# Performance work log

Measured on AMD Instinct MI355X. Metric: run time of the kernel, lower is better.

The kernel has to match this reference:

```python
import jax, jax.numpy as jnp
import numpy as np

N_NODES = 100000
N_RELS = 4
N_EDGES = 250000  # per relation
D = 128


def setup_inputs() -> dict:
    key = jax.random.key(0)
    ks = jax.random.split(key, 7)
    scale = 1.0 / np.sqrt(D)  # xavier-like scaling for stability
    x = jax.random.normal(ks[0], (N_NODES, D), dtype=jnp.float32)
    weight = jax.random.normal(ks[1], (N_RELS, D, D), dtype=jnp.float32) * scale
    conv_bias = jax.random.normal(ks[2], (N_RELS, D), dtype=jnp.float32) * 0.1
    loop_weight = jax.random.normal(ks[3], (D, D), dtype=jnp.float32) * scale
    node_bias = jax.random.normal(ks[4], (1, D), dtype=jnp.float32) * 0.1
    src = jax.random.randint(ks[5], (N_RELS, N_EDGES), 0, N_NODES)
    dst = jax.random.randint(ks[6], (N_RELS, N_EDGES), 0, N_NODES)
    return {"x": x, "weight": weight, "conv_bias": conv_bias,
            "loop_weight": loop_weight, "node_bias": node_bias,
            "src": src, "dst": dst}


def reference(x, weight, conv_bias, loop_weight, node_bias, src, dst):
    N = x.shape[0]

    def per_rel(s, d, W, b):
        # GraphConv(norm='right'): sum src feats into dst, divide by in-degree (clamped to 1),
        # then matmul weight (aggregate-first since in_feat == out_feat), add bias, activation.
        msg = jax.ops.segment_sum(x[s], d, num_segments=N)              # [N, D]
        deg = jax.ops.segment_sum(jnp.ones(s.shape, x.dtype), d, num_segments=N)
        h = (msg / jnp.maximum(deg, 1.0)[:, None]) @ W + b              # [N, D]
        return jax.nn.relu(h)

    hs = jax.vmap(per_rel)(src, dst, weight, conv_bias)                 # [R, N, D]
    h = hs.mean(axis=0)                                                 # HeteroGraphConv aggregate='mean'
    h = h * jax.nn.sigmoid(h)                                           # GLU(tile(h, 2)) == SiLU(h)
    h = h + x @ loop_weight + node_bias                                  # self-loop + ntype bias
    return jax.nn.relu(h)                                                # dropout=0 (eval)
```

## Files before the change

kernel.cpp:

```cpp
#include <hip/hip_runtime.h>
#include <hip/hip_bf16.h>

#define N_NODES 100000
#define N_RELS  4
#define N_EDGES 250000
#define TOTAL_E (N_RELS * N_EDGES)
#define NR      (N_RELS * N_NODES)
#define D       128

typedef __attribute__((ext_vector_type(8))) short bf16x8;
typedef __attribute__((ext_vector_type(4))) float f32x4;

__device__ __forceinline__ float b2f(short u) {
    unsigned int x = ((unsigned int)(unsigned short)u) << 16;
    return __builtin_bit_cast(float, x);
}
__device__ __forceinline__ unsigned short f2b(float f) {
    unsigned int u = __builtin_bit_cast(unsigned int, f);
    return (unsigned short)((u + 0x7fffu + ((u >> 16) & 1u)) >> 16);
}

__global__ __launch_bounds__(256) void hist_kernel(
    const int* __restrict__ dst, int* __restrict__ deg, int total)
{
    int i = blockIdx.x * 256 + threadIdx.x;
    if (i >= total) return;
    int rel = i / N_EDGES;
    atomicAdd(&deg[rel * N_NODES + dst[i]], 1);
}

__global__ __launch_bounds__(256) void scan1_kernel(
    const int* __restrict__ in, int* __restrict__ out,
    int* __restrict__ aux, int n)
{
    __shared__ int s[256];
    int t = threadIdx.x;
    int base = blockIdx.x * 1024 + t * 4;
    int v[4];
    int sum = 0;
    #pragma unroll
    for (int j = 0; j < 4; ++j) {
        v[j] = (base + j < n) ? in[base + j] : 0;
        sum += v[j];
    }
    s[t] = sum;
    for (int off = 1; off < 256; off <<= 1) {
        __syncthreads();
        int u = (t >= off) ? s[t - off] : 0;
        __syncthreads();
        s[t] += u;
    }
    __syncthreads();
    int excl = (t > 0) ? s[t - 1] : 0;
    #pragma unroll
    for (int j = 0; j < 4; ++j) {
        if (base + j < n) out[base + j] = excl;
        excl += v[j];
    }
    if (t == 255) aux[blockIdx.x] = s[255];
}

__global__ __launch_bounds__(512) void scan2_kernel(int* __restrict__ aux, int n)
{
    __shared__ int s[512];
    int t = threadIdx.x;
    s[t] = (t < n) ? aux[t] : 0;
    for (int off = 1; off < 512; off <<= 1) {
        __syncthreads();
        int u = (t >= off) ? s[t - off] : 0;
        __syncthreads();
        s[t] += u;
    }
    __syncthreads();
    int excl = (t > 0) ? s[t - 1] : 0;
    if (t < n) aux[t] = excl;
}

__global__ __launch_bounds__(256) void addoff_kernel(
    int* __restrict__ off, int* __restrict__ cursor,
    const int* __restrict__ aux, int n)
{
    int i = blockIdx.x * 256 + threadIdx.x;
    if (i >= n) return;
    int v = off[i] + aux[i >> 10];
    off[i] = v;
    cursor[i] = v;
}

__global__ __launch_bounds__(256) void fill_kernel(
    const int* __restrict__ dst, const int* __restrict__ src,
    int* __restrict__ cursor, int* __restrict__ sorted_src, int total)
{
    int i = blockIdx.x * 256 + threadIdx.x;
    if (i >= total) return;
    int rel = i / N_EDGES;
    int pos = atomicAdd(&cursor[rel * N_NODES + dst[i]], 1);
    sorted_src[pos] = src[i];
}

__global__ __launch_bounds__(256) void convert_x_kernel(
    const float* __restrict__ x, unsigned short* __restrict__ xb, int total8)
{
    int i = blockIdx.x * 256 + threadIdx.x;
    if (i >= total8) return;
    float4 v0 = *reinterpret_cast<const float4*>(x + (size_t)i * 8);
    float4 v1 = *reinterpret_cast<const float4*>(x + (size_t)i * 8 + 4);
    bf16x8 o;
    o[0] = (short)f2b(v0.x); o[1] = (short)f2b(v0.y);
    o[2] = (short)f2b(v0.z); o[3] = (short)f2b(v0.w);
    o[4] = (short)f2b(v1.x); o[5] = (short)f2b(v1.y);
    o[6] = (short)f2b(v1.z); o[7] = (short)f2b(v1.w);
    *reinterpret_cast<bf16x8*>(xb + (size_t)i * 8) = o;
}

__global__ __launch_bounds__(256) void convert_w_kernel(
    const float* __restrict__ weight,
    const float* __restrict__ loop_w,
    unsigned short* __restrict__ wT)
{
    int i = blockIdx.x * 256 + threadIdx.x;
    if (i >= 5 * D * D) return;
    int mat = i >> 14;
    int n   = (i >> 7) & 127;
    int k   = i & 127;
    const float* srcm = (mat < 4) ? (weight + (size_t)mat * D * D) : loop_w;
    wT[i] = f2b(srcm[k * D + n]);
}

__global__ __launch_bounds__(256) void fused_gemm_mfma(
    const unsigned short* __restrict__ xb,
    const unsigned short* __restrict__ wT,
    const float* __restrict__ conv_bias,
    const float* __restrict__ node_bias,
    const int* __restrict__ deg,
    const int* __restrict__ off,
    const int* __restrict__ sorted_src,
    float* __restrict__ out)
{
    __shared__ __align__(16) unsigned char sIn[32 * 256];

    const int tid  = threadIdx.x;
    const int row0 = blockIdx.x * 32;
    const int wid  = tid >> 6;
    const int lane = tid & 63;
    const int l15  = lane & 15;
    const int l4   = lane >> 4;
    const int swA  = (l15 & 7) << 4;

    const int gr = tid >> 3;
    const int gc = tid & 7;
    const int gsw = (gr & 7) << 4;

    f32x4 acc_mean[2][2];
    f32x4 acc_self[2][2];
    #pragma unroll
    for (int m = 0; m < 2; ++m)
        #pragma unroll
        for (int n = 0; n < 2; ++n)
            acc_mean[m][n] = (f32x4){0.f, 0.f, 0.f, 0.f};

    for (int phase = 0; phase < 5; ++phase) {
        __syncthreads();

        if (phase < 4) {
            int node = row0 + gr;
            int dgi  = deg[phase * N_NODES + node];
            int beg  = off[phase * N_NODES + node];
            float a[16];
            #pragma unroll
            for (int j = 0; j < 16; ++j) a[j] = 0.f;
            const int* sp = sorted_src + beg;
            for (int e = 0; e < dgi; ++e) {
                const unsigned short* xp = xb + (size_t)sp[e] * D + gc * 16;
                bf16x8 v0 = *reinterpret_cast<const bf16x8*>(xp);
                bf16x8 v1 = *reinterpret_cast<const bf16x8*>(xp + 8);
                #pragma unroll
                for (int j = 0; j < 8; ++j) {
                    a[j]     += b2f(v0[j]);
                    a[8 + j] += b2f(v1[j]);
                }
            }
            float scale = 1.0f / fmaxf((float)dgi, 1.0f);
            bf16x8 o0, o1;
            #pragma unroll
            for (int j = 0; j < 8; ++j) {
                o0[j] = (short)f2b(a[j] * scale);
                o1[j] = (short)f2b(a[8 + j] * scale);
            }
            int base = gr * 256;
            *reinterpret_cast<bf16x8*>(&sIn[base + ((gc * 32) ^ gsw)])      = o0;
            *reinterpret_cast<bf16x8*>(&sIn[base + ((gc * 32 + 16) ^ gsw)]) = o1;
        } else {
            #pragma unroll
            for (int t = 0; t < 2; ++t) {
                int id = tid + t * 256;
                int r  = id >> 4;
                int kb = (id & 15) * 16;
                bf16x8 v = *reinterpret_cast<const bf16x8*>(
                    xb + (size_t)(row0 + r) * D + kb / 2);
                *reinterpret_cast<bf16x8*>(&sIn[r * 256 + (kb ^ ((r & 7) << 4))]) = v;
            }
        }
        __syncthreads();

        const unsigned short* wp = wT + (size_t)phase * D * D;
        bf16x8 bfr[2][4];
        #pragma unroll
        for (int n = 0; n < 2; ++n)
            #pragma unroll
            for (int s = 0; s < 4; ++s) {
                int col = wid * 32 + n * 16 + l15;
                bfr[n][s] = *reinterpret_cast<const bf16x8*>(
                    wp + col * D + s * 32 + l4 * 8);
            }

        f32x4 acc[2][2];
        #pragma unroll
        for (int m = 0; m < 2; ++m)
            #pragma unroll
            for (int n = 0; n < 2; ++n)
                acc[m][n] = (f32x4){0.f, 0.f, 0.f, 0.f};

        #pragma unroll
        for (int s = 0; s < 4; ++s) {
            int kb = s * 64 + l4 * 16;
            bf16x8 a0 = *reinterpret_cast<const bf16x8*>(
                &sIn[l15 * 256 + (kb ^ swA)]);
            bf16x8 a1 = *reinterpret_cast<const bf16x8*>(
                &sIn[(16 + l15) * 256 + (kb ^ swA)]);
            acc[0][0] = __builtin_amdgcn_mfma_f32_16x16x32_bf16(a0, bfr[0][s], acc[0][0], 0, 0, 0);
            acc[0][1] = __builtin_amdgcn_mfma_f32_16x16x32_bf16(a0, bfr[1][s], acc[0][1], 0, 0, 0);
            acc[1][0] = __builtin_amdgcn_mfma_f32_16x16x32_bf16(a1, bfr[0][s], acc[1][0], 0, 0, 0);
            acc[1][1] = __builtin_amdgcn_mfma_f32_16x16x32_bf16(a1, bfr[1][s], acc[1][1], 0, 0, 0);
        }

        if (phase < 4) {
            float b0 = conv_bias[phase * D + wid * 32 + l15];
            float b1 = conv_bias[phase * D + wid * 32 + 16 + l15];
            #pragma unroll
            for (int m = 0; m < 2; ++m)
                #pragma unroll
                for (int j = 0; j < 4; ++j) {
                    acc_mean[m][0][j] += 0.25f * fmaxf(acc[m][0][j] + b0, 0.f);
                    acc_mean[m][1][j] += 0.25f * fmaxf(acc[m][1][j] + b1, 0.f);
                }
        } else {
            float b0 = node_bias[wid * 32 + l15];
            float b1 = node_bias[wid * 32 + 16 + l15];
            #pragma unroll
            for (int m = 0; m < 2; ++m)
                #pragma unroll
                for (int j = 0; j < 4; ++j) {
                    acc_self[m][0][j] = acc[m][0][j] + b0;
                    acc_self[m][1][j] = acc[m][1][j] + b1;
                }
        }
    }

    #pragma unroll
    for (int m = 0; m < 2; ++m)
        #pragma unroll
        for (int n = 0; n < 2; ++n)
            #pragma unroll
            for (int j = 0; j < 4; ++j) {
                float mn = acc_mean[m][n][j];
                float sl = mn / (1.0f + __expf(-mn));
                float v  = fmaxf(sl + acc_self[m][n][j], 0.f);
                int row = row0 + m * 16 + l4 * 4 + j;
                int col = wid * 32 + n * 16 + l15;
                out[(size_t)row * D + col] = v;
            }
}

extern "C" void kernel_launch(void* const* d_in, const int* in_sizes, int n_in,
                              void* d_out, int out_size, void* d_ws, size_t ws_size,
                              hipStream_t stream) {
    const float* x         = (const float*)d_in[0];
    const float* weight    = (const float*)d_in[1];
    const float* conv_bias = (const float*)d_in[2];
    const float* loop_w    = (const float*)d_in[3];
    const float* node_bias = (const float*)d_in[4];
    const int*   src       = (const int*)d_in[5];
    const int*   dst       = (const int*)d_in[6];
    float* out = (float*)d_out;

    char* w = (char*)d_ws;
    int* deg                  = (int*)(w);
    int* off                  = (int*)(w + 1600000);
    int* cursor               = (int*)(w + 3200000);
    int* aux                  = (int*)(w + 4800000);
    int* sorted_src           = (int*)(w + 4802048);
    unsigned short* xb        = (unsigned short*)(w + 8802048);
    unsigned short* wT        = (unsigned short*)(w + 8802048 + (size_t)N_NODES * D * 2);

    const int SCAN_BLKS = (NR + 1023) / 1024;

    convert_x_kernel<<<(N_NODES * D / 8 + 255) / 256, 256, 0, stream>>>(
        x, xb, N_NODES * D / 8);
    convert_w_kernel<<<(5 * D * D + 255) / 256, 256, 0, stream>>>(
        weight, loop_w, wT);

    hipMemsetAsync(deg, 0, NR * sizeof(int), stream);
    hist_kernel<<<(TOTAL_E + 255) / 256, 256, 0, stream>>>(dst, deg, TOTAL_E);
    scan1_kernel<<<SCAN_BLKS, 256, 0, stream>>>(deg, off, aux, NR);
    scan2_kernel<<<1, 512, 0, stream>>>(aux, SCAN_BLKS);
    addoff_kernel<<<(NR + 255) / 256, 256, 0, stream>>>(off, cursor, aux, NR);
    fill_kernel<<<(TOTAL_E + 255) / 256, 256, 0, stream>>>(dst, src, cursor,
                                                           sorted_src, TOTAL_E);

    fused_gemm_mfma<<<N_NODES / 32, 256, 0, stream>>>(
        xb, wT, conv_bias, node_bias, deg, off, sorted_src, out);
}
```

Measured before the change: 355.4 us.

## Merge prep kernels, fold scan passes, and gather edges per block with LDS atomics

Folds the x/weight conversion and the degree histogram into one prep kernel. It also drops the separate second scan kernel by having each block reduce the preceding block sums itself. The fill step now packs the source index with the destination's low 5 bits. This lets the fused kernel spread a 32-node tile's edges evenly over all threads and accumulate them into an fp32 LDS tile with shared-memory atomics, replacing the per-node serial loops that suffered load imbalance. Weight fragments are now loaded from global memory inside the MFMA loop rather than hoisted, and the self-loop GEMM reads x directly from global memory. The LDS float atomics and the larger shared footprint may contend or reduce occupancy.

```diff
diff --git a/kernel.cpp b/kernel.cpp
--- a/kernel.cpp
+++ b/kernel.cpp
@@ -20,13 +20,40 @@
     return (unsigned short)((u + 0x7fffu + ((u >> 16) & 1u)) >> 16);
 }
 
-__global__ __launch_bounds__(256) void hist_kernel(
-    const int* __restrict__ dst, int* __restrict__ deg, int total)
-{
-    int i = blockIdx.x * 256 + threadIdx.x;
-    if (i >= total) return;
-    int rel = i / N_EDGES;
-    atomicAdd(&deg[rel * N_NODES + dst[i]], 1);
+#define PREP_X_BLKS 6250
+#define PREP_W_BLKS 320
+#define PREP_H_BLKS 3907
+__global__ __launch_bounds__(256) void prep_kernel(
+    const float* __restrict__ x, const float* __restrict__ weight,
+    const float* __restrict__ loop_w, const int* __restrict__ dst,
+    unsigned short* __restrict__ xb, unsigned short* __restrict__ wT,
+    int* __restrict__ deg)
+{
+    int b = blockIdx.x, t = threadIdx.x;
+    if (b < PREP_X_BLKS) {
+        int i = b * 256 + t;
+        float4 v0 = *reinterpret_cast<const float4*>(x + (size_t)i * 8);
+        float4 v1 = *reinterpret_cast<const float4*>(x + (size_t)i * 8 + 4);
+        bf16x8 o;
+        o[0] = (short)f2b(v0.x); o[1] = (short)f2b(v0.y);
+        o[2] = (short)f2b(v0.z); o[3] = (short)f2b(v0.w);
+        o[4] = (short)f2b(v1.x); o[5] = (short)f2b(v1.y);
+        o[6] = (short)f2b(v1.z); o[7] = (short)f2b(v1.w);
+        *reinterpret_cast<bf16x8*>(xb + (size_t)i * 8) = o;
+    } else if (b < PREP_X_BLKS + PREP_W_BLKS) {
+        int i = (b - PREP_X_BLKS) * 256 + t;
+        int mat = i >> 14;
+        int n   = (i >> 7) & 127;
+        int k   = i & 127;
+        const float* srcm = (mat < 4) ? (weight + (size_t)mat * D * D) : loop_w;
+        wT[i] = f2b(srcm[k * D + n]);
+    } else {
+        int i = (b - PREP_X_BLKS - PREP_W_BLKS) * 256 + t;
+        if (i < TOTAL_E) {
+            int rel = i / N_EDGES;
+            atomicAdd(&deg[rel * N_NODES + dst[i]], 1);
+        }
+    }
 }
 
 __global__ __launch_bounds__(256) void scan1_kernel(
@@ -60,71 +87,39 @@
     if (t == 255) aux[blockIdx.x] = s[255];
 }
 
-__global__ __launch_bounds__(512) void scan2_kernel(int* __restrict__ aux, int n)
-{
-    __shared__ int s[512];
-    int t = threadIdx.x;
-    s[t] = (t < n) ? aux[t] : 0;
-    for (int off = 1; off < 512; off <<= 1) {
-        __syncthreads();
-        int u = (t >= off) ? s[t - off] : 0;
-        __syncthreads();
-        s[t] += u;
-    }
-    __syncthreads();
-    int excl = (t > 0) ? s[t - 1] : 0;
-    if (t < n) aux[t] = excl;
-}
-
-__global__ __launch_bounds__(256) void addoff_kernel(
+__global__ __launch_bounds__(256) void addoff2_kernel(
     int* __restrict__ off, int* __restrict__ cursor,
     const int* __restrict__ aux, int n)
 {
-    int i = blockIdx.x * 256 + threadIdx.x;
-    if (i >= n) return;
-    int v = off[i] + aux[i >> 10];
-    off[i] = v;
-    cursor[i] = v;
-}
-
-__global__ __launch_bounds__(256) void fill_kernel(
+    __shared__ int sred[256];
+    int c = blockIdx.x, t = threadIdx.x;
+    int part = 0;
+    for (int j = t; j < c; j += 256) part += aux[j];
+    sred[t] = part;
+    for (int o = 128; o > 0; o >>= 1) {
+        __syncthreads();
+        if (t < o) sred[t] += sred[t + o];
+    }
+    __syncthreads();
+    int S = sred[0];
+    int base = c * 1024 + t * 4;
+    #pragma unroll
+    for (int j = 0; j < 4; ++j) {
+        int i = base + j;
+        if (i < n) { int v = off[i] + S; off[i] = v; cursor[i] = v; }
+    }
+}
+
+__global__ __launch_bounds__(256) void fill_pack_kernel(
     const int* __restrict__ dst, const int* __restrict__ src,
-    int* __restrict__ cursor, int* __restrict__ sorted_src, int total)
+    int* __restrict__ cursor, unsigned int* __restrict__ sorted_pack, int total)
 {
     int i = blockIdx.x * 256 + threadIdx.x;
     if (i >= total) return;
     int rel = i / N_EDGES;
-    int pos = atomicAdd(&cursor[rel * N_NODES + dst[i]], 1);
-    sorted_src[pos] = src[i];
-}
-
-__global__ __launch_bounds__(256) void convert_x_kernel(
-    const float* __restrict__ x, unsigned short* __restrict__ xb, int total8)
-{
-    int i = blockIdx.x * 256 + threadIdx.x;
-    if (i >= total8) return;
-    float4 v0 = *reinterpret_cast<const float4*>(x + (size_t)i * 8);
-    float4 v1 = *reinterpret_cast<const float4*>(x + (size_t)i * 8 + 4);
-    bf16x8 o;
-    o[0] = (short)f2b(v0.x); o[1] = (short)f2b(v0.y);
-    o[2] = (short)f2b(v0.z); o[3] = (short)f2b(v0.w);
-    o[4] = (short)f2b(v1.x); o[5] = (short)f2b(v1.y);
-    o[6] = (short)f2b(v1.z); o[7] = (short)f2b(v1.w);
-    *reinterpret_cast<bf16x8*>(xb + (size_t)i * 8) = o;
-}
-
-__global__ __launch_bounds__(256) void convert_w_kernel(
-    const float* __restrict__ weight,
-    const float* __restrict__ loop_w,
-    unsigned short* __restrict__ wT)
-{
-    int i = blockIdx.x * 256 + threadIdx.x;
-    if (i >= 5 * D * D) return;
-    int mat = i >> 14;
-    int n   = (i >> 7) & 127;
-    int k   = i & 127;
-    const float* srcm = (mat < 4) ? (weight + (size_t)mat * D * D) : loop_w;
-    wT[i] = f2b(srcm[k * D + n]);
+    int d = dst[i];
+    int pos = atomicAdd(&cursor[rel * N_NODES + d], 1);
+    sorted_pack[pos] = (unsigned int)src[i] | ((unsigned int)(d & 31) << 17);
 }
 
 __global__ __launch_bounds__(256) void fused_gemm_mfma(
@@ -134,9 +129,10 @@
     const float* __restrict__ node_bias,
     const int* __restrict__ deg,
     const int* __restrict__ off,
-    const int* __restrict__ sorted_src,
+    const unsigned int* __restrict__ spack,
     float* __restrict__ out)
 {
+    __shared__ float tileF[32 * 128];
     __shared__ __align__(16) unsigned char sIn[32 * 256];
 
     const int tid  = threadIdx.x;
@@ -147,9 +143,12 @@
     const int l4   = lane >> 4;
     const int swA  = (l15 & 7) << 4;
 
-    const int gr = tid >> 3;
-    const int gc = tid & 7;
-    const int gsw = (gr & 7) << 4;
+    const int glc = lane & 15;
+    const int gew = lane >> 4;
+
+    const int nr = tid >> 3;
+    const int nc = (tid & 7) * 16;
+    const int nsw = (nr & 7) << 4;
 
     f32x4 acc_mean[2][2];
     f32x4 acc_self[2][2];
@@ -159,61 +158,59 @@
         for (int n = 0; n < 2; ++n)
             acc_mean[m][n] = (f32x4){0.f, 0.f, 0.f, 0.f};
 
-    for (int phase = 0; phase < 5; ++phase) {
-        __syncthreads();
-
-        if (phase < 4) {
-            int node = row0 + gr;
-            int dgi  = deg[phase * N_NODES + node];
-            int beg  = off[phase * N_NODES + node];
-            float a[16];
-            #pragma unroll
-            for (int j = 0; j < 16; ++j) a[j] = 0.f;
-            const int* sp = sorted_src + beg;
-            for (int e = 0; e < dgi; ++e) {
-                const unsigned short* xp = xb + (size_t)sp[e] * D + gc * 16;
-                bf16x8 v0 = *reinterpret_cast<const bf16x8*>(xp);
-                bf16x8 v1 = *reinterpret_cast<const bf16x8*>(xp + 8);
+    for (int phase = 0; phase < 4; ++phase) {
+        __syncthreads();
+        #pragma unroll
+        for (int k = 0; k < 4; ++k)
+            *reinterpret_cast<f32x4*>(&tileF[tid * 16 + k * 4]) =
+                (f32x4){0.f, 0.f, 0.f, 0.f};
+        __syncthreads();
+
+        {
+            int ebeg = off[phase * N_NODES + row0];
+            int eidx = phase * N_NODES + row0 + 32;
+            int eend = (eidx < NR) ? off[eidx] : TOTAL_E;
+            for (int e = ebeg + wid * 4 + gew; e < eend; e += 16) {
+                unsigned int pk = spack[e];
+                int srcn = pk & 0x1FFFF;
+                int lrow = (pk >> 17) & 31;
+                bf16x8 v = *reinterpret_cast<const bf16x8*>(
+                    xb + (size_t)srcn * D + glc * 8);
+                char* base = (char*)tileF + lrow * 512;
+                int sw = (lrow & 7) << 4;
                 #pragma unroll
                 for (int j = 0; j < 8; ++j) {
-                    a[j]     += b2f(v0[j]);
-                    a[8 + j] += b2f(v1[j]);
+                    int boff = (glc * 32 + j * 4) ^ sw;
+                    atomicAdd(reinterpret_cast<float*>(base + boff), b2f(v[j]));
                 }
             }
-            float scale = 1.0f / fmaxf((float)dgi, 1.0f);
-            bf16x8 o0, o1;
-            #pragma unroll
-            for (int j = 0; j < 8; ++j) {
-                o0[j] = (short)f2b(a[j] * scale);
-                o1[j] = (short)f2b(a[8 + j] * scale);
-            }
-            int base = gr * 256;
-            *reinterpret_cast<bf16x8*>(&sIn[base + ((gc * 32) ^ gsw)])      = o0;
-            *reinterpret_cast<bf16x8*>(&sIn[base + ((gc * 32 + 16) ^ gsw)]) = o1;
-        } else {
-            #pragma unroll
-            for (int t = 0; t < 2; ++t) {
-                int id = tid + t * 256;
-                int r  = id >> 4;
-                int kb = (id & 15) * 16;
-                bf16x8 v = *reinterpret_cast<const bf16x8*>(
-                    xb + (size_t)(row0 + r) * D + kb / 2);
-                *reinterpret_cast<bf16x8*>(&sIn[r * 256 + (kb ^ ((r & 7) << 4))]) = v;
+        }
+        __syncthreads();
+
+        {
+            int dg = deg[phase * N_NODES + row0 + nr];
+            float scl = 1.0f / fmaxf((float)dg, 1.0f);
+            float vals[16];
+            #pragma unroll
+            for (int k = 0; k < 4; ++k) {
+                f32x4 q = *reinterpret_cast<const f32x4*>(
+                    (char*)tileF + nr * 512 + (((tid & 7) * 64 + k * 16) ^ nsw));
+                vals[k * 4 + 0] = q.x * scl; vals[k * 4 + 1] = q.y * scl;
+                vals[k * 4 + 2] = q.z * scl; vals[k * 4 + 3] = q.w * scl;
+            }
+            #pragma unroll
+            for (int k = 0; k < 2; ++k) {
+                bf16x8 o;
+                #pragma unroll
+                for (int j = 0; j < 8; ++j)
+                    o[j] = (short)f2b(vals[k * 8 + j]);
+                *reinterpret_cast<bf16x8*>(
+                    &sIn[nr * 256 + (((tid & 7) * 32 + k * 16) ^ nsw)]) = o;
             }
         }
         __syncthreads();
 
         const unsigned short* wp = wT + (size_t)phase * D * D;
-        bf16x8 bfr[2][4];
-        #pragma unroll
-        for (int n = 0; n < 2; ++n)
-            #pragma unroll
-            for (int s = 0; s < 4; ++s) {
-                int col = wid * 32 + n * 16 + l15;
-                bfr[n][s] = *reinterpret_cast<const bf16x8*>(
-                    wp + col * D + s * 32 + l4 * 8);
-            }
-
         f32x4 acc[2][2];
         #pragma unroll
         for (int m = 0; m < 2; ++m)
@@ -228,33 +225,60 @@
                 &sIn[l15 * 256 + (kb ^ swA)]);
             bf16x8 a1 = *reinterpret_cast<const bf16x8*>(
                 &sIn[(16 + l15) * 256 + (kb ^ swA)]);
-            acc[0][0] = __builtin_amdgcn_mfma_f32_16x16x32_bf16(a0, bfr[0][s], acc[0][0], 0, 0, 0);
-            acc[0][1] = __builtin_amdgcn_mfma_f32_16x16x32_bf16(a0, bfr[1][s], acc[0][1], 0, 0, 0);
-            acc[1][0] = __builtin_amdgcn_mfma_f32_16x16x32_bf16(a1, bfr[0][s], acc[1][0], 0, 0, 0);
-            acc[1][1] = __builtin_amdgcn_mfma_f32_16x16x32_bf16(a1, bfr[1][s], acc[1][1], 0, 0, 0);
-        }
-
-        if (phase < 4) {
-            float b0 = conv_bias[phase * D + wid * 32 + l15];
-            float b1 = conv_bias[phase * D + wid * 32 + 16 + l15];
-            #pragma unroll
-            for (int m = 0; m < 2; ++m)
-                #pragma unroll
-                for (int j = 0; j < 4; ++j) {
-                    acc_mean[m][0][j] += 0.25f * fmaxf(acc[m][0][j] + b0, 0.f);
-                    acc_mean[m][1][j] += 0.25f * fmaxf(acc[m][1][j] + b1, 0.f);
-                }
-        } else {
-            float b0 = node_bias[wid * 32 + l15];
-            float b1 = node_bias[wid * 32 + 16 + l15];
-            #pragma unroll
-            for (int m = 0; m < 2; ++m)
-                #pragma unroll
-                for (int j = 0; j < 4; ++j) {
-                    acc_self[m][0][j] = acc[m][0][j] + b0;
-                    acc_self[m][1][j] = acc[m][1][j] + b1;
-                }
-        }
+            bf16x8 b0 = *reinterpret_cast<const bf16x8*>(
+                wp + (wid * 32 + l15) * D + s * 32 + l4 * 8);
+            bf16x8 b1 = *reinterpret_cast<const bf16x8*>(
+                wp + (wid * 32 + 16 + l15) * D + s * 32 + l4 * 8);
+            acc[0][0] = __builtin_amdgcn_mfma_f32_16x16x32_bf16(a0, b0, acc[0][0], 0, 0, 0);
+            acc[0][1] = __builtin_amdgcn_mfma_f32_16x16x32_bf16(a0, b1, acc[0][1], 0, 0, 0);
+            acc[1][0] = __builtin_amdgcn_mfma_f32_16x16x32_bf16(a1, b0, acc[1][0], 0, 0, 0);
+            acc[1][1] = __builtin_amdgcn_mfma_f32_16x16x32_bf16(a1, b1, acc[1][1], 0, 0, 0);
+        }
+
+        float b0 = conv_bias[phase * D + wid * 32 + l15];
+        float b1 = conv_bias[phase * D + wid * 32 + 16 + l15];
+        #pragma unroll
+        for (int m = 0; m < 2; ++m)
+            #pragma unroll
+            for (int j = 0; j < 4; ++j) {
+                acc_mean[m][0][j] += 0.25f * fmaxf(acc[m][0][j] + b0, 0.f);
+                acc_mean[m][1][j] += 0.25f * fmaxf(acc[m][1][j] + b1, 0.f);
+            }
+    }
+
+    {
+        const unsigned short* wp = wT + (size_t)4 * D * D;
+        f32x4 acc[2][2];
+        #pragma unroll
+        for (int m = 0; m < 2; ++m)
+            #pragma unroll
+            for (int n = 0; n < 2; ++n)
+                acc[m][n] = (f32x4){0.f, 0.f, 0.f, 0.f};
+
+        #pragma unroll
+        for (int s = 0; s < 4; ++s) {
+            bf16x8 a0 = *reinterpret_cast<const bf16x8*>(
+                xb + (size_t)(row0 + l15) * D + s * 32 + l4 * 8);
+            bf16x8 a1 = *reinterpret_cast<const bf16x8*>(
+                xb + (size_t)(row0 + 16 + l15) * D + s * 32 + l4 * 8);
+            bf16x8 b0 = *reinterpret_cast<const bf16x8*>(
+                wp + (wid * 32 + l15) * D + s * 32 + l4 * 8);
+            bf16x8 b1 = *reinterpret_cast<const bf16x8*>(
+                wp + (wid * 32 + 16 + l15) * D + s * 32 + l4 * 8);
+            acc[0][0] = __builtin_amdgcn_mfma_f32_16x16x32_bf16(a0, b0, acc[0][0], 0, 0, 0);
+            acc[0][1] = __builtin_amdgcn_mfma_f32_16x16x32_bf16(a0, b1, acc[0][1], 0, 0, 0);
+            acc[1][0] = __builtin_amdgcn_mfma_f32_16x16x32_bf16(a1, b0, acc[1][0], 0, 0, 0);
+            acc[1][1] = __builtin_amdgcn_mfma_f32_16x16x32_bf16(a1, b1, acc[1][1], 0, 0, 0);
+        }
+        float b0 = node_bias[wid * 32 + l15];
+        float b1 = node_bias[wid * 32 + 16 + l15];
+        #pragma unroll
+        for (int m = 0; m < 2; ++m)
+            #pragma unroll
+            for (int j = 0; j < 4; ++j) {
+                acc_self[m][0][j] = acc[m][0][j] + b0;
+                acc_self[m][1][j] = acc[m][1][j] + b1;
+            }
     }
 
     #pragma unroll
@@ -289,25 +313,19 @@
     int* off                  = (int*)(w + 1600000);
     int* cursor               = (int*)(w + 3200000);
     int* aux                  = (int*)(w + 4800000);
-    int* sorted_src           = (int*)(w + 4802048);
+    unsigned int* spack       = (unsigned int*)(w + 4802048);
     unsigned short* xb        = (unsigned short*)(w + 8802048);
     unsigned short* wT        = (unsigned short*)(w + 8802048 + (size_t)N_NODES * D * 2);
 
     const int SCAN_BLKS = (NR + 1023) / 1024;
 
-    convert_x_kernel<<<(N_NODES * D / 8 + 255) / 256, 256, 0, stream>>>(
-        x, xb, N_NODES * D / 8);
-    convert_w_kernel<<<(5 * D * D + 255) / 256, 256, 0, stream>>>(
-        weight, loop_w, wT);
-
     hipMemsetAsync(deg, 0, NR * sizeof(int), stream);
-    hist_kernel<<<(TOTAL_E + 255) / 256, 256, 0, stream>>>(dst, deg, TOTAL_E);
+    prep_kernel<<<PREP_X_BLKS + PREP_W_BLKS + PREP_H_BLKS, 256, 0, stream>>>(
+        x, weight, loop_w, dst, xb, wT, deg);
     scan1_kernel<<<SCAN_BLKS, 256, 0, stream>>>(deg, off, aux, NR);
-    scan2_kernel<<<1, 512, 0, stream>>>(aux, SCAN_BLKS);
-    addoff_kernel<<<(NR + 255) / 256, 256, 0, stream>>>(off, cursor, aux, NR);
-    fill_kernel<<<(TOTAL_E + 255) / 256, 256, 0, stream>>>(dst, src, cursor,
-                                                           sorted_src, TOTAL_E);
-
+    addoff2_kernel<<<SCAN_BLKS, 256, 0, stream>>>(off, cursor, aux, NR);
+    fill_pack_kernel<<<(TOTAL_E + 255) / 256, 256, 0, stream>>>(
+        dst, src, cursor, spack, TOTAL_E);
     fused_gemm_mfma<<<N_NODES / 32, 256, 0, stream>>>(
-        xb, wT, conv_bias, node_bias, deg, off, sorted_src, out);
-}
+        xb, wT, conv_bias, node_bias, deg, off, spack, out);
+}
```

After: 917.5 us. 2.58x slower.
